# Optimization experiments

Hardware: AMD Instinct MI355X
Metric: run time of the kernel (lower is better)

The kernel has to match this reference:

```python
import jax, jax.numpy as jnp
import numpy as np

OUTERCUTOFF = 5.0  # seqm_parameters['pair_outer_cutoff']
LENGTH_CONV = 1.8897261258369282  # Angstrom -> Bohr (constants.length_conversion_factor)
NMOL, MOLSIZE = 1024, 128


def setup_inputs() -> dict:
    key = jax.random.key(0)
    k1, k2 = jax.random.split(key)
    species = jax.random.randint(k1, (NMOL, MOLSIZE), 0, 9).astype(jnp.int32)
    coordinates = jax.random.uniform(k2, (NMOL, MOLSIZE, 3), dtype=jnp.float32) * 20.0
    # core charges indexed by atomic number (0=blank, H=1, ..., F=9)
    tore = jnp.array([0.0, 1.0, 0.0, 1.0, 2.0, 3.0, 4.0, 5.0, 6.0, 7.0], dtype=jnp.float32)
    return {"species": species, "coordinates": coordinates, "tore": tore}


def reference(species, coordinates, tore):
    nmol, molsize = species.shape
    nonblank = species > 0                               # (nmol, molsize)
    flat_nb = nonblank.reshape(-1)
    atom_index = jnp.arange(nmol * molsize, dtype=jnp.int32)
    real_atoms = atom_index[flat_nb]                     # compaction (eager, data-dependent)
    n_real = real_atoms.shape[0]
    inv_real_atoms = jnp.zeros((nmol * molsize,), jnp.int32).at[real_atoms].set(
        jnp.arange(n_real, dtype=jnp.int32))
    Z = species.reshape(-1)[real_atoms]
    nHeavy = jnp.sum(species > 1, axis=1)
    nHydro = jnp.sum(species == 1, axis=1)
    nocc = (jnp.sum(tore[species], axis=1) / 2.0).reshape(-1).astype(jnp.int32)
    t1 = (jnp.arange(molsize, dtype=jnp.int32) * (molsize + 1))[None, :]
    t2 = (jnp.arange(nmol, dtype=jnp.int32) * molsize ** 2)[:, None]
    maskd = (t1 + t2).reshape(-1)[real_atoms]
    atom_molid = jnp.repeat(jnp.arange(nmol, dtype=jnp.int32), molsize)[flat_nb]
    # pair bookkeeping: [i, a, b] with first=atom a, second=atom b
    nonblank_pairs = (nonblank[:, None, :] & nonblank[:, :, None]).reshape(-1)
    ai = atom_index.reshape(nmol, molsize)
    pair_first = jnp.broadcast_to(ai[:, :, None], (nmol, molsize, molsize)).reshape(-1)
    pair_second = jnp.broadcast_to(ai[:, None, :], (nmol, molsize, molsize)).reshape(-1)
    # paircoord_raw[i, a, b] = coord[i, b] - coord[i, a]
    paircoord_raw = (coordinates[:, None, :, :] - coordinates[:, :, None, :]).reshape(-1, 3)
    pairdist_raw = jnp.linalg.norm(paircoord_raw, axis=1)
    close_pairs = pairdist_raw < OUTERCUTOFF
    pairs = (pair_first < pair_second) & nonblank_pairs & close_pairs
    pidx = jnp.where(pairs)[0]
    paircoord = paircoord_raw[pidx]
    pairdist = pairdist_raw[pidx]
    rij = pairdist * LENGTH_CONV
    idxi = inv_real_atoms[pair_first[pidx]]
    idxj = inv_real_atoms[pair_second[pidx]]
    ni = Z[idxi]
    nj = Z[idxj]
    xij = paircoord / pairdist[:, None]
    mask = real_atoms[idxi] * molsize + real_atoms[idxj] % molsize
    pair_molid = atom_molid[idxi]
    return (nmol, molsize, nHeavy, nHydro, nocc, Z, maskd, atom_molid,
            mask, pair_molid, ni, nj, idxi, idxj, xij, rij)
```

## Files before the change

### kernel.cpp

```cpp
#include <hip/hip_runtime.h>

#define NMOL 1024
#define MOLSIZE 128


__device__ __forceinline__ float pair_dist(float ax, float ay, float az,
                                           float bx, float by, float bz,
                                           float& dx, float& dy, float& dz) {
    dx = __fsub_rn(bx, ax);
    dy = __fsub_rn(by, ay);
    dz = __fsub_rn(bz, az);
    float d2 = __fadd_rn(__fadd_rn(__fmul_rn(dx, dx), __fmul_rn(dy, dy)), __fmul_rn(dz, dz));
    return __fsqrt_rn(d2);
}

__global__ __launch_bounds__(256, 4) void k_fused(const int* __restrict__ species,
                                                  const float* __restrict__ coord,
                                                  const float* __restrict__ tore,
                                                  float* __restrict__ out,
                                                  unsigned int* __restrict__ pub) {
    __shared__ float cx[MOLSIZE], cy[MOLSIZE], cz[MOLSIZE], spf[MOLSIZE];
    __shared__ int iv[MOLSIZE];
    __shared__ unsigned long long bal_s[256];
    __shared__ int sIncl[256];
    __shared__ int sH[2], sY[2], sN[2];
    __shared__ float sT[2];
    __shared__ int wpair[4], wtot[4];
    __shared__ int redALT[4], redAALL[4], redPLT[4], redPALL[4];
    __shared__ int wc0s;

    int m = blockIdx.x, t = threadIdx.x;
    int lane = t & 63, w = t >> 6;

    int s_at = 0;
    unsigned long long amb = 0ull;
    if (t < MOLSIZE) {
        int f = m * MOLSIZE + t;
        s_at = species[f];
        bool nb = (s_at > 0);
        float x = coord[3 * f + 0], y = coord[3 * f + 1], z = coord[3 * f + 2];
        float sent = 1.0e30f * (float)(t + 1);
        cx[t] = nb ? x : sent;
        cy[t] = nb ? y : sent;
        cz[t] = nb ? z : sent;
        spf[t] = (float)s_at;
        amb = __ballot(nb);
        if (t == 0) wc0s = __popcll(amb);
        int h = (s_at > 1) ? 1 : 0, yy = (s_at == 1) ? 1 : 0, nn = nb ? 1 : 0;
        float tv = tore[s_at];
        for (int d = 32; d > 0; d >>= 1) {
            h += __shfl_down(h, d);
            yy += __shfl_down(yy, d);
            nn += __shfl_down(nn, d);
            tv += __shfl_down(tv, d);
        }
        if (lane == 0) { sH[w] = h; sY[w] = yy; sN[w] = nn; sT[w] = tv; }
    }
    __syncthreads();
    if (t == 0) {
        out[2 + m] = (float)(sH[0] + sH[1]);
        out[2 + NMOL + m] = (float)(sY[0] + sY[1]);
        out[2 + 2 * NMOL + m] = (float)((int)((sT[0] + sT[1]) * 0.5f));
        if (m == 0) { out[0] = (float)NMOL; out[1] = (float)MOLSIZE; }
    }

    float bxl = cx[lane], byl = cy[lane], bzl = cz[lane];
    float bxh = cx[64 + lane], byh = cy[64 + lane], bzh = cz[64 + lane];
    int wcount = 0;
    for (int j = 0; j < 32; ++j) {
        int a = w + 4 * j;
        float ax = cx[a], ay = cy[a], az = cz[a];
        unsigned long long mb0 = 0ull, mb1 = 0ull;
        if (a < 63) {
            float dx, dy, dz;
            float dist = pair_dist(ax, ay, az, bxl, byl, bzl, dx, dy, dz);
            mb0 = __ballot((lane > a) && (dist < 5.0f));
        }
        if (a < 127) {
            float dx, dy, dz;
            float dist = pair_dist(ax, ay, az, bxh, byh, bzh, dx, dy, dz);
            mb1 = __ballot(((64 + lane) > a) && (dist < 5.0f));
        }
        if (lane == 0) { bal_s[2 * a] = mb0; bal_s[2 * a + 1] = mb1; }
        wcount += __popcll(mb0) + __popcll(mb1);
    }
    if (lane == 0) wpair[w] = wcount;
    __syncthreads();

    if (t == 0) {
        unsigned int nreal = (unsigned int)(sN[0] + sN[1]);
        unsigned int ptot = (unsigned int)(wpair[0] + wpair[1] + wpair[2] + wpair[3]);
        __hip_atomic_store(&pub[m], 0x80000000u | (ptot << 8) | nreal,
                           __ATOMIC_RELAXED, __HIP_MEMORY_SCOPE_AGENT);
    }

    unsigned long long bal = bal_s[t];
    int v = __popcll(bal);
    for (int d = 1; d < 64; d <<= 1) {
        int u = __shfl_up(v, d);
        if (lane >= d) v += u;
    }
    if (lane == 63) wtot[w] = v;
    if (t < MOLSIZE && s_at > 0)
        iv[t] = __popcll(amb & ((1ull << lane) - 1ull)) + ((w == 1) ? wc0s : 0);
    __syncthreads();
    int add = 0;
    for (int ww = 0; ww < w; ++ww) add += wtot[ww];
    sIncl[t] = v + add;

    unsigned int pw[4];
#pragma unroll
    for (int k = 0; k < 4; ++k) {
        unsigned int val = __hip_atomic_load(&pub[4 * t + k], __ATOMIC_RELAXED,
                                             __HIP_MEMORY_SCOPE_AGENT);
        while (!(val & 0x80000000u)) {
            __builtin_amdgcn_s_sleep(1);
            val = __hip_atomic_load(&pub[4 * t + k], __ATOMIC_RELAXED,
                                    __HIP_MEMORY_SCOPE_AGENT);
        }
        pw[k] = val;
    }
    int aLT = 0, aALL = 0, pLT = 0, pALL = 0;
    int i0 = 4 * t;
#pragma unroll
    for (int k = 0; k < 4; ++k) {
        int real = (int)(pw[k] & 0xFFu);
        int pr = (int)((pw[k] >> 8) & 0x1FFFu);
        aALL += real;
        pALL += pr;
        if (i0 + k < m) { aLT += real; pLT += pr; }
    }
    for (int d = 32; d > 0; d >>= 1) {
        aLT += __shfl_down(aLT, d);
        aALL += __shfl_down(aALL, d);
        pLT += __shfl_down(pLT, d);
        pALL += __shfl_down(pALL, d);
    }
    if (lane == 0) { redALT[w] = aLT; redAALL[w] = aALL; redPLT[w] = pLT; redPALL[w] = pALL; }
    __syncthreads();

    int mol_base = redALT[0] + redALT[1] + redALT[2] + redALT[3];
    int n_real   = redAALL[0] + redAALL[1] + redAALL[2] + redAALL[3];
    int qbase    = redPLT[0] + redPLT[1] + redPLT[2] + redPLT[3];
    int npairs   = redPALL[0] + redPALL[1] + redPALL[2] + redPALL[3];

    if (t < MOLSIZE && s_at > 0) {
        int g = mol_base + iv[t];
        out[3074 + g] = spf[t];
        out[3074 + n_real + g] = (float)(t * (MOLSIZE + 1) + m * (MOLSIZE * MOLSIZE));
        out[3074 + 2 * n_real + g] = (float)m;
    }
    int np_mol = sIncl[255];

    int offP = 3074 + 3 * n_real;
    float* pm0 = out + offP;
    float* pm1 = pm0 + npairs;
    float* pm2 = pm1 + npairs;
    float* pm3 = pm2 + npairs;
    float* pm4 = pm3 + npairs;
    float* pm5 = pm4 + npairs;
    float* px  = pm5 + npairs;
    float* pr  = px + 3 * npairs;
    float fm = (float)m;

    for (int q = t; q < np_mol; q += 256) {
        int c = 0;
        if (sIncl[c + 127] <= q) c += 128;
        if (sIncl[c + 63] <= q) c += 64;
        if (sIncl[c + 31] <= q) c += 32;
        if (sIncl[c + 15] <= q) c += 16;
        if (sIncl[c + 7] <= q) c += 8;
        if (sIncl[c + 3] <= q) c += 4;
        if (sIncl[c + 1] <= q) c += 2;
        if (sIncl[c] <= q) c += 1;
        int r = q - (c ? sIncl[c - 1] : 0);
        unsigned long long mb = bal_s[c];
        unsigned int cur = (unsigned int)mb;
        int idx = 0;
        int cc = __popc(cur);
        if (r >= cc) { r -= cc; idx = 32; cur = (unsigned int)(mb >> 32); }
        cc = __popc(cur & 0xFFFFu); if (r >= cc) { r -= cc; idx += 16; cur >>= 16; }
        cc = __popc(cur & 0xFFu);   if (r >= cc) { r -= cc; idx += 8;  cur >>= 8; }
        cc = __popc(cur & 0xFu);    if (r >= cc) { r -= cc; idx += 4;  cur >>= 4; }
        cc = __popc(cur & 0x3u);    if (r >= cc) { r -= cc; idx += 2;  cur >>= 2; }
        cc = cur & 1u;              if (r >= cc) { idx += 1; }
        int a = c >> 1;
        int b = ((c & 1) << 6) | idx;
        float dx, dy, dz;
        float dist = pair_dist(cx[a], cy[a], cz[a], cx[b], cy[b], cz[b], dx, dy, dz);
        int Q = qbase + q;
        pm0[Q] = (float)(m * (MOLSIZE * MOLSIZE) + a * MOLSIZE + b);
        pm1[Q] = fm;
        pm2[Q] = spf[a];
        pm3[Q] = spf[b];
        pm4[Q] = (float)(mol_base + iv[a]);
        pm5[Q] = (float)(mol_base + iv[b]);
        px[3 * Q + 0] = __fdiv_rn(dx, dist);
        px[3 * Q + 1] = __fdiv_rn(dy, dist);
        px[3 * Q + 2] = __fdiv_rn(dz, dist);
        pr[Q] = __fmul_rn(dist, 1.8897261258369282f);
    }
}

extern "C" void kernel_launch(void* const* d_in, const int* in_sizes, int n_in,
                              void* d_out, int out_size, void* d_ws, size_t ws_size,
                              hipStream_t stream) {
    const int* species = (const int*)d_in[0];
    const float* coords = (const float*)d_in[1];
    const float* tore = (const float*)d_in[2];
    float* out = (float*)d_out;
    unsigned int* pub = (unsigned int*)d_ws;

    hipMemsetAsync(pub, 0, NMOL * sizeof(unsigned int), stream);
    k_fused<<<NMOL, 256, 0, stream>>>(species, coords, tore, out, pub);
}
```

Measured before the change: 84.31 us.

## Pack four molecules per 1024-thread block and share published counts via LDS

Each block now handles four molecules with 1024 threads, launching 256 blocks instead of 1024. Each thread polls one published molecule entry rather than four. The decoded counts are staged in shared memory so all four molecule groups in the block can reuse them for their prefix sums, cutting global spin-polling traffic and grid-wide barrier contention. The cost is larger blocks with more shared memory and block-wide syncs coupling four molecules, plus the requirement that all 256 blocks be co-resident to avoid deadlock.

```diff
diff --git a/kernel.cpp b/kernel.cpp
--- a/kernel.cpp
+++ b/kernel.cpp
@@ -2,6 +2,8 @@
 
 #define NMOL 1024
 #define MOLSIZE 128
+#define MPB 4
+#define NBLK (NMOL / MPB)
 
 
 __device__ __forceinline__ float pair_dist(float ax, float ay, float az,
@@ -14,38 +16,43 @@
     return __fsqrt_rn(d2);
 }
 
-__global__ __launch_bounds__(256, 4) void k_fused(const int* __restrict__ species,
-                                                  const float* __restrict__ coord,
-                                                  const float* __restrict__ tore,
-                                                  float* __restrict__ out,
-                                                  unsigned int* __restrict__ pub) {
-    __shared__ float cx[MOLSIZE], cy[MOLSIZE], cz[MOLSIZE], spf[MOLSIZE];
-    __shared__ int iv[MOLSIZE];
-    __shared__ unsigned long long bal_s[256];
-    __shared__ int sIncl[256];
-    __shared__ int sH[2], sY[2], sN[2];
-    __shared__ float sT[2];
-    __shared__ int wpair[4], wtot[4];
-    __shared__ int redALT[4], redAALL[4], redPLT[4], redPALL[4];
-    __shared__ int wc0s;
-
-    int m = blockIdx.x, t = threadIdx.x;
-    int lane = t & 63, w = t >> 6;
+__global__ __launch_bounds__(1024) void k_fused(const int* __restrict__ species,
+                                                const float* __restrict__ coord,
+                                                const float* __restrict__ tore,
+                                                float* __restrict__ out,
+                                                unsigned int* __restrict__ pub) {
+    __shared__ float cx[MPB][MOLSIZE], cy[MPB][MOLSIZE], cz[MPB][MOLSIZE], spf[MPB][MOLSIZE];
+    __shared__ int iv[MPB][MOLSIZE];
+    __shared__ unsigned long long bal_s[MPB][256];
+    __shared__ int sIncl[MPB][256];
+    __shared__ int sH[MPB][2], sY[MPB][2], sN[MPB][2];
+    __shared__ float sT[MPB][2];
+    __shared__ int wpair[MPB][4], wtot[MPB][4];
+    __shared__ int redALT[MPB][4], redAALL[MPB][4], redPLT[MPB][4], redPALL[MPB][4];
+    __shared__ int wc0s[MPB];
+    __shared__ int pubR[NMOL], pubP[NMOL];
+
+    int t = threadIdx.x;
+    int g = t >> 8;
+    int u = t & 255;
+    int m = blockIdx.x * MPB + g;
+    int lane = t & 63;
+    int wl = (t >> 6) & 3;
 
     int s_at = 0;
     unsigned long long amb = 0ull;
-    if (t < MOLSIZE) {
-        int f = m * MOLSIZE + t;
+    if (u < MOLSIZE) {
+        int f = m * MOLSIZE + u;
         s_at = species[f];
         bool nb = (s_at > 0);
         float x = coord[3 * f + 0], y = coord[3 * f + 1], z = coord[3 * f + 2];
-        float sent = 1.0e30f * (float)(t + 1);
-        cx[t] = nb ? x : sent;
-        cy[t] = nb ? y : sent;
-        cz[t] = nb ? z : sent;
-        spf[t] = (float)s_at;
+        float sent = 1.0e30f * (float)(u + 1);
+        cx[g][u] = nb ? x : sent;
+        cy[g][u] = nb ? y : sent;
+        cz[g][u] = nb ? z : sent;
+        spf[g][u] = (float)s_at;
         amb = __ballot(nb);
-        if (t == 0) wc0s = __popcll(amb);
+        if (u == 0) wc0s[g] = __popcll(amb);
         int h = (s_at > 1) ? 1 : 0, yy = (s_at == 1) ? 1 : 0, nn = nb ? 1 : 0;
         float tv = tore[s_at];
         for (int d = 32; d > 0; d >>= 1) {
@@ -54,22 +61,22 @@
             nn += __shfl_down(nn, d);
             tv += __shfl_down(tv, d);
         }
-        if (lane == 0) { sH[w] = h; sY[w] = yy; sN[w] = nn; sT[w] = tv; }
-    }
-    __syncthreads();
-    if (t == 0) {
-        out[2 + m] = (float)(sH[0] + sH[1]);
-        out[2 + NMOL + m] = (float)(sY[0] + sY[1]);
-        out[2 + 2 * NMOL + m] = (float)((int)((sT[0] + sT[1]) * 0.5f));
+        if (lane == 0) { sH[g][wl] = h; sY[g][wl] = yy; sN[g][wl] = nn; sT[g][wl] = tv; }
+    }
+    __syncthreads();
+    if (u == 0) {
+        out[2 + m] = (float)(sH[g][0] + sH[g][1]);
+        out[2 + NMOL + m] = (float)(sY[g][0] + sY[g][1]);
+        out[2 + 2 * NMOL + m] = (float)((int)((sT[g][0] + sT[g][1]) * 0.5f));
         if (m == 0) { out[0] = (float)NMOL; out[1] = (float)MOLSIZE; }
     }
 
-    float bxl = cx[lane], byl = cy[lane], bzl = cz[lane];
-    float bxh = cx[64 + lane], byh = cy[64 + lane], bzh = cz[64 + lane];
+    float bxl = cx[g][lane], byl = cy[g][lane], bzl = cz[g][lane];
+    float bxh = cx[g][64 + lane], byh = cy[g][64 + lane], bzh = cz[g][64 + lane];
     int wcount = 0;
     for (int j = 0; j < 32; ++j) {
-        int a = w + 4 * j;
-        float ax = cx[a], ay = cy[a], az = cz[a];
+        int a = wl + 4 * j;
+        float ax = cx[g][a], ay = cy[g][a], az = cz[g][a];
         unsigned long long mb0 = 0ull, mb1 = 0ull;
         if (a < 63) {
             float dx, dy, dz;
@@ -81,76 +88,78 @@
             float dist = pair_dist(ax, ay, az, bxh, byh, bzh, dx, dy, dz);
             mb1 = __ballot(((64 + lane) > a) && (dist < 5.0f));
         }
-        if (lane == 0) { bal_s[2 * a] = mb0; bal_s[2 * a + 1] = mb1; }
+        if (lane == 0) { bal_s[g][2 * a] = mb0; bal_s[g][2 * a + 1] = mb1; }
         wcount += __popcll(mb0) + __popcll(mb1);
     }
-    if (lane == 0) wpair[w] = wcount;
-    __syncthreads();
-
-    if (t == 0) {
-        unsigned int nreal = (unsigned int)(sN[0] + sN[1]);
-        unsigned int ptot = (unsigned int)(wpair[0] + wpair[1] + wpair[2] + wpair[3]);
+    if (lane == 0) wpair[g][wl] = wcount;
+    __syncthreads();
+
+    if (u == 0) {
+        unsigned int nreal = (unsigned int)(sN[g][0] + sN[g][1]);
+        unsigned int ptot =
+            (unsigned int)(wpair[g][0] + wpair[g][1] + wpair[g][2] + wpair[g][3]);
         __hip_atomic_store(&pub[m], 0x80000000u | (ptot << 8) | nreal,
                            __ATOMIC_RELAXED, __HIP_MEMORY_SCOPE_AGENT);
     }
 
-    unsigned long long bal = bal_s[t];
+    unsigned long long bal = bal_s[g][u];
     int v = __popcll(bal);
     for (int d = 1; d < 64; d <<= 1) {
-        int u = __shfl_up(v, d);
-        if (lane >= d) v += u;
-    }
-    if (lane == 63) wtot[w] = v;
-    if (t < MOLSIZE && s_at > 0)
-        iv[t] = __popcll(amb & ((1ull << lane) - 1ull)) + ((w == 1) ? wc0s : 0);
+        int uu = __shfl_up(v, d);
+        if (lane >= d) v += uu;
+    }
+    if (lane == 63) wtot[g][wl] = v;
+    if (u < MOLSIZE && s_at > 0)
+        iv[g][u] = __popcll(amb & ((1ull << lane) - 1ull)) + ((wl == 1) ? wc0s[g] : 0);
     __syncthreads();
     int add = 0;
-    for (int ww = 0; ww < w; ++ww) add += wtot[ww];
-    sIncl[t] = v + add;
-
-    unsigned int pw[4];
-#pragma unroll
-    for (int k = 0; k < 4; ++k) {
-        unsigned int val = __hip_atomic_load(&pub[4 * t + k], __ATOMIC_RELAXED,
+    for (int ww = 0; ww < wl; ++ww) add += wtot[g][ww];
+    sIncl[g][u] = v + add;
+
+    {
+        unsigned int val = __hip_atomic_load(&pub[t], __ATOMIC_RELAXED,
                                              __HIP_MEMORY_SCOPE_AGENT);
         while (!(val & 0x80000000u)) {
-            __builtin_amdgcn_s_sleep(1);
-            val = __hip_atomic_load(&pub[4 * t + k], __ATOMIC_RELAXED,
+            __builtin_amdgcn_s_sleep(2);
+            val = __hip_atomic_load(&pub[t], __ATOMIC_RELAXED,
                                     __HIP_MEMORY_SCOPE_AGENT);
         }
-        pw[k] = val;
-    }
-    int aLT = 0, aALL = 0, pLT = 0, pALL = 0;
-    int i0 = 4 * t;
-#pragma unroll
-    for (int k = 0; k < 4; ++k) {
-        int real = (int)(pw[k] & 0xFFu);
-        int pr = (int)((pw[k] >> 8) & 0x1FFFu);
-        aALL += real;
-        pALL += pr;
-        if (i0 + k < m) { aLT += real; pLT += pr; }
-    }
+        pubR[t] = (int)(val & 0xFFu);
+        pubP[t] = (int)((val >> 8) & 0x1FFFu);
+    }
+    __syncthreads();
+
+    int4 ca = ((const int4*)pubR)[u];
+    int4 cp = ((const int4*)pubP)[u];
+    int i0 = 4 * u;
+    int aLT = ((i0 + 0) < m ? ca.x : 0) + ((i0 + 1) < m ? ca.y : 0) +
+              ((i0 + 2) < m ? ca.z : 0) + ((i0 + 3) < m ? ca.w : 0);
+    int aALL = ca.x + ca.y + ca.z + ca.w;
+    int pLT = ((i0 + 0) < m ? cp.x : 0) + ((i0 + 1) < m ? cp.y : 0) +
+              ((i0 + 2) < m ? cp.z : 0) + ((i0 + 3) < m ? cp.w : 0);
+    int pALL = cp.x + cp.y + cp.z + cp.w;
     for (int d = 32; d > 0; d >>= 1) {
         aLT += __shfl_down(aLT, d);
         aALL += __shfl_down(aALL, d);
         pLT += __shfl_down(pLT, d);
         pALL += __shfl_down(pALL, d);
     }
-    if (lane == 0) { redALT[w] = aLT; redAALL[w] = aALL; redPLT[w] = pLT; redPALL[w] = pALL; }
-    __syncthreads();
-
-    int mol_base = redALT[0] + redALT[1] + redALT[2] + redALT[3];
-    int n_real   = redAALL[0] + redAALL[1] + redAALL[2] + redAALL[3];
-    int qbase    = redPLT[0] + redPLT[1] + redPLT[2] + redPLT[3];
-    int npairs   = redPALL[0] + redPALL[1] + redPALL[2] + redPALL[3];
-
-    if (t < MOLSIZE && s_at > 0) {
-        int g = mol_base + iv[t];
-        out[3074 + g] = spf[t];
-        out[3074 + n_real + g] = (float)(t * (MOLSIZE + 1) + m * (MOLSIZE * MOLSIZE));
-        out[3074 + 2 * n_real + g] = (float)m;
-    }
-    int np_mol = sIncl[255];
+    if (lane == 0) { redALT[g][wl] = aLT; redAALL[g][wl] = aALL;
+                     redPLT[g][wl] = pLT; redPALL[g][wl] = pALL; }
+    __syncthreads();
+
+    int mol_base = redALT[g][0] + redALT[g][1] + redALT[g][2] + redALT[g][3];
+    int n_real   = redAALL[g][0] + redAALL[g][1] + redAALL[g][2] + redAALL[g][3];
+    int qbase    = redPLT[g][0] + redPLT[g][1] + redPLT[g][2] + redPLT[g][3];
+    int npairs   = redPALL[g][0] + redPALL[g][1] + redPALL[g][2] + redPALL[g][3];
+
+    if (u < MOLSIZE && s_at > 0) {
+        int gi = mol_base + iv[g][u];
+        out[3074 + gi] = spf[g][u];
+        out[3074 + n_real + gi] = (float)(u * (MOLSIZE + 1) + m * (MOLSIZE * MOLSIZE));
+        out[3074 + 2 * n_real + gi] = (float)m;
+    }
+    int np_mol = sIncl[g][255];
 
     int offP = 3074 + 3 * n_real;
     float* pm0 = out + offP;
@@ -163,18 +172,18 @@
     float* pr  = px + 3 * npairs;
     float fm = (float)m;
 
-    for (int q = t; q < np_mol; q += 256) {
+    for (int q = u; q < np_mol; q += 256) {
         int c = 0;
-        if (sIncl[c + 127] <= q) c += 128;
-        if (sIncl[c + 63] <= q) c += 64;
-        if (sIncl[c + 31] <= q) c += 32;
-        if (sIncl[c + 15] <= q) c += 16;
-        if (sIncl[c + 7] <= q) c += 8;
-        if (sIncl[c + 3] <= q) c += 4;
-        if (sIncl[c + 1] <= q) c += 2;
-        if (sIncl[c] <= q) c += 1;
-        int r = q - (c ? sIncl[c - 1] : 0);
-        unsigned long long mb = bal_s[c];
+        if (sIncl[g][c + 127] <= q) c += 128;
+        if (sIncl[g][c + 63] <= q) c += 64;
+        if (sIncl[g][c + 31] <= q) c += 32;
+        if (sIncl[g][c + 15] <= q) c += 16;
+        if (sIncl[g][c + 7] <= q) c += 8;
+        if (sIncl[g][c + 3] <= q) c += 4;
+        if (sIncl[g][c + 1] <= q) c += 2;
+        if (sIncl[g][c] <= q) c += 1;
+        int r = q - (c ? sIncl[g][c - 1] : 0);
+        unsigned long long mb = bal_s[g][c];
         unsigned int cur = (unsigned int)mb;
         int idx = 0;
         int cc = __popc(cur);
@@ -187,14 +196,15 @@
         int a = c >> 1;
         int b = ((c & 1) << 6) | idx;
         float dx, dy, dz;
-        float dist = pair_dist(cx[a], cy[a], cz[a], cx[b], cy[b], cz[b], dx, dy, dz);
+        float dist = pair_dist(cx[g][a], cy[g][a], cz[g][a],
+                               cx[g][b], cy[g][b], cz[g][b], dx, dy, dz);
         int Q = qbase + q;
         pm0[Q] = (float)(m * (MOLSIZE * MOLSIZE) + a * MOLSIZE + b);
         pm1[Q] = fm;
-        pm2[Q] = spf[a];
-        pm3[Q] = spf[b];
-        pm4[Q] = (float)(mol_base + iv[a]);
-        pm5[Q] = (float)(mol_base + iv[b]);
+        pm2[Q] = spf[g][a];
+        pm3[Q] = spf[g][b];
+        pm4[Q] = (float)(mol_base + iv[g][a]);
+        pm5[Q] = (float)(mol_base + iv[g][b]);
         px[3 * Q + 0] = __fdiv_rn(dx, dist);
         px[3 * Q + 1] = __fdiv_rn(dy, dist);
         px[3 * Q + 2] = __fdiv_rn(dz, dist);
@@ -212,5 +222,5 @@
     unsigned int* pub = (unsigned int*)d_ws;
 
     hipMemsetAsync(pub, 0, NMOL * sizeof(unsigned int), stream);
-    k_fused<<<NMOL, 256, 0, stream>>>(species, coords, tore, out, pub);
+    k_fused<<<NBLK, 1024, 0, stream>>>(species, coords, tore, out, pub);
 }
```

Result: faster. 79.39 us (-5.8%).
